# Kernel optimization log

Hardware: AMD Instinct MI355X
Metric: run time of the kernel (lower is better)

Reference implementation:

```python
import jax, jax.numpy as jnp
import numpy as np

WAY, NQ, C, FS = 5, 4096, 64, 5
T = FS * FS            # 25 spatial tokens
EMB = T + 1            # feature_size**2 + feature_proj_dim = 26
HEADS = 2
HD = EMB // HEADS      # 13
SCALE = HD ** -0.5
T_ATTN = 5.0           # args.temperature_attn
TEMP = 0.2             # args.temperature
LN_EPS = 1e-6


def _ln(x, g, b):
    m = x.mean(-1, keepdims=True)
    v = jnp.mean((x - m) ** 2, axis=-1, keepdims=True)
    return (x - m) / jnp.sqrt(v + LN_EPS) * g + b


def _block(x, p):
    # pre-LN transformer block (timm-style), x: (B, T, EMB)
    h = _ln(x, p['ln1_g'], p['ln1_b'])
    qkv = h @ p['qkv_w'].T + p['qkv_b']                       # (B,T,3*EMB)
    B, N, _ = qkv.shape
    qkv = qkv.reshape(B, N, 3, HEADS, HD).transpose(2, 0, 3, 1, 4)
    q, k, v = qkv[0], qkv[1], qkv[2]                          # (B,H,T,hd)
    a = jax.nn.softmax(jnp.einsum('bhqd,bhkd->bhqk', q, k) * SCALE, axis=-1)
    o = jnp.einsum('bhqk,bhkd->bhqd', a, v).transpose(0, 2, 1, 3).reshape(B, N, EMB)
    x = x + o @ p['attn_w'].T + p['attn_b']
    h = _ln(x, p['ln2_g'], p['ln2_b'])
    h = jax.nn.gelu(h @ p['fc1_w'].T + p['fc1_b'], approximate=False)
    return x + h @ p['fc2_w'].T + p['fc2_b']


def _decoder(corr, src, tgt, p):
    # CATs TransformerAggregator, num_hyperpixel=1, depth=1
    # corr: (B,1,T,T); src/tgt: (B,1,T,1) projected features
    pos = jnp.concatenate([
        jnp.broadcast_to(p['pos_x'], (1, 1, FS, FS, EMB // 2)),
        jnp.broadcast_to(p['pos_y'], (1, 1, FS, FS, EMB // 2))], axis=-1).reshape(1, 1, T, EMB)
    B = corr.shape[0]
    x = jnp.concatenate([jnp.swapaxes(corr, -1, -2), tgt], axis=3) + pos
    x = _block(x.reshape(B, T, EMB), p)
    x = (x @ p['dec_w'].T + p['dec_b']).reshape(B, 1, T, T)
    x = jnp.swapaxes(x, -1, -2) + corr            # swap axes for second self-attn pass
    x = jnp.concatenate([x, src], axis=3) + pos
    x = _block(x.reshape(B, T, EMB), p)           # same block weights reused
    x = (x @ p['dec_w'].T + p['dec_b']).reshape(B, 1, T, T) + corr
    return x.mean(axis=1)                         # (B,T,T)


def _forward(spt, qry, proj_w, proj_b, pos_x, pos_y, ln1_g, ln1_b, qkv_w, qkv_b,
             attn_w, attn_b, ln2_g, ln2_b, fc1_w, fc1_b, fc2_w, fc2_b, dec_w, dec_b):
    p = dict(pos_x=pos_x, pos_y=pos_y, ln1_g=ln1_g, ln1_b=ln1_b, qkv_w=qkv_w,
             qkv_b=qkv_b, attn_w=attn_w, attn_b=attn_b, ln2_g=ln2_g, ln2_b=ln2_b,
             fc1_w=fc1_w, fc1_b=fc1_b, fc2_w=fc2_w, fc2_b=fc2_b, dec_w=dec_w, dec_b=dec_b)
    # normalize_feature: subtract channel mean
    spt = spt - spt.mean(axis=1, keepdims=True)
    qry = qry - qry.mean(axis=1, keepdims=True)
    spt_f = jnp.broadcast_to(spt[None], (NQ, WAY, C, FS, FS)).reshape(-1, C, FS, FS)
    qry_f = jnp.broadcast_to(qry[:, None], (NQ, WAY, C, FS, FS)).reshape(-1, C, FS, FS)

    def l2n(x):  # FeatureL2Norm over channel dim
        return x / jnp.sqrt(jnp.sum(x * x, axis=1, keepdims=True) + 1e-6)

    s = l2n(spt_f).reshape(-1, C, T)
    t = l2n(qry_f).reshape(-1, C, T)
    corr = jnp.einsum('bci,bcj->bij', s, t)[:, None]                  # (B,1,T,T)
    sp = (jnp.swapaxes(spt_f.reshape(-1, C, T), 1, 2) @ proj_w.T + proj_b)[:, None]
    tp = (jnp.swapaxes(qry_f.reshape(-1, C, T), 1, 2) @ proj_w.T + proj_b)[:, None]
    refined = _decoder(corr, sp, tp, p)                               # (B,T,T)

    corr_s = refined.reshape(NQ, WAY, T, FS, FS)
    corr_q = refined.reshape(NQ, WAY, FS, FS, T)

    def gnorm(x, axis):  # torch.var is unbiased (ddof=1)
        m = x.mean(axis=axis, keepdims=True)
        v = jnp.var(x, axis=axis, keepdims=True, ddof=1)
        return (x - m) / jnp.sqrt(v + 1e-5)

    corr_s = jax.nn.softmax(gnorm(corr_s, 2) / T_ATTN, axis=2).reshape(NQ, WAY, FS, FS, FS, FS)
    corr_q = jax.nn.softmax(gnorm(corr_q, 4) / T_ATTN, axis=4).reshape(NQ, WAY, FS, FS, FS, FS)
    attn_s = corr_s.sum(axis=(4, 5))                                  # (NQ,WAY,FS,FS)
    attn_q = corr_q.sum(axis=(2, 3))
    spt_att = attn_s[:, :, None] * spt[None]                          # (NQ,WAY,C,FS,FS)
    qry_att = attn_q[:, :, None] * qry[:, None]
    sp_p = spt_att.mean(axis=(-1, -2))                                # (NQ,WAY,C)
    qp_p = qry_att.mean(axis=(-1, -2))
    n1 = jnp.maximum(jnp.linalg.norm(sp_p, axis=-1), 1e-8)
    n2 = jnp.maximum(jnp.linalg.norm(qp_p, axis=-1), 1e-8)
    sim = jnp.sum(sp_p * qp_p, axis=-1) / (n1 * n2)                   # (NQ,WAY)
    return sim / TEMP


def setup_inputs() -> dict:
    key = jax.random.key(0)
    ks = jax.random.split(key, 12)

    def w(i, shape, s=0.02):
        return jax.random.normal(ks[i], shape, jnp.float32) * s

    return {
        'spt': jax.random.normal(ks[0], (WAY, C, FS, FS), jnp.float32),
        'qry': jax.random.normal(ks[1], (NQ, C, FS, FS), jnp.float32),
        'proj_w': w(2, (1, C)), 'proj_b': jnp.zeros((1,), jnp.float32),
        'pos_x': w(3, (1, 1, 1, FS, EMB // 2)),
        'pos_y': w(4, (1, 1, FS, 1, EMB // 2)),
        'ln1_g': jnp.ones((EMB,), jnp.float32), 'ln1_b': jnp.zeros((EMB,), jnp.float32),
        'qkv_w': w(5, (3 * EMB, EMB)), 'qkv_b': jnp.zeros((3 * EMB,), jnp.float32),
        'attn_w': w(6, (EMB, EMB)), 'attn_b': jnp.zeros((EMB,), jnp.float32),
        'ln2_g': jnp.ones((EMB,), jnp.float32), 'ln2_b': jnp.zeros((EMB,), jnp.float32),
        'fc1_w': w(7, (4 * EMB, EMB)), 'fc1_b': jnp.zeros((4 * EMB,), jnp.float32),
        'fc2_w': w(8, (EMB, 4 * EMB)), 'fc2_b': jnp.zeros((EMB,), jnp.float32),
        'dec_w': w(9, (T, EMB)), 'dec_b': jnp.zeros((T,), jnp.float32),
    }


def reference(spt, qry, proj_w, proj_b, pos_x, pos_y, ln1_g, ln1_b, qkv_w, qkv_b,
              attn_w, attn_b, ln2_g, ln2_b, fc1_w, fc1_b, fc2_w, fc2_b, dec_w, dec_b):
    return _forward(spt, qry, proj_w, proj_b, pos_x, pos_y, ln1_g, ln1_b, qkv_w, qkv_b,
                    attn_w, attn_b, ln2_g, ln2_b, fc1_w, fc1_b, fc2_w, fc2_b, dec_w, dec_b)
```

## Files before the change

### kernel.cpp

```cpp
#include <hip/hip_runtime.h>
#include <math.h>

#define WAYS 5
#define NQN 4096
#define NBATCH (NQN*WAYS)
#define SAB 68

#define WS_SC 0
#define WS_RS 8000
#define WS_SP 8125
#define WS_QM 8250
#define WS_QR 110650
#define WS_TP 213050

#define P_L1G 0
#define P_L1B 26
#define P_L2G 52
#define P_L2B 78
#define P_QKVB 104
#define P_ATTB 182
#define P_FC1B 208
#define P_FC2B 312
#define P_DECB 338
#define P_TOT 363

__global__ void prep_spt(const float* __restrict__ spt, const float* __restrict__ proj_w,
                         const float* __restrict__ proj_b, float* __restrict__ ws) {
    int tid = threadIdx.x;
    if (tid >= 125) return;
    int w = tid / 25, i = tid % 25;
    const float* base = spt + w * 1600 + i;
    float s = 0.f;
    for (int c = 0; c < 64; c++) s += base[c * 25];
    float m = s * (1.f / 64.f);
    float ss = 0.f, pj = 0.f;
    for (int c = 0; c < 64; c++) {
        float v = base[c * 25] - m;
        ss += v * v; pj += v * proj_w[c];
        ws[WS_SC + (w * 25 + i) * 64 + c] = v;
    }
    ws[WS_RS + w * 25 + i] = rsqrtf(ss + 1e-6f);
    ws[WS_SP + w * 25 + i] = pj + proj_b[0];
}

__global__ void prep_qry(const float* __restrict__ qry, const float* __restrict__ proj_w,
                         const float* __restrict__ proj_b, float* __restrict__ ws) {
    int idx = blockIdx.x * 256 + threadIdx.x;
    if (idx >= NQN * 25) return;
    int q = idx / 25, j = idx % 25;
    const float* base = qry + q * 1600 + j;
    float s = 0.f;
    for (int c = 0; c < 64; c++) s += base[c * 25];
    float m = s * (1.f / 64.f);
    float ss = 0.f, pj = 0.f;
    for (int c = 0; c < 64; c++) {
        float v = base[c * 25] - m;
        ss += v * v; pj += v * proj_w[c];
    }
    ws[WS_QM + idx] = m;
    ws[WS_QR + idx] = rsqrtf(ss + 1e-6f);
    ws[WS_TP + idx] = pj + proj_b[0];
}

template<int M, int N, int K, int TM, int TN, int SA, int WN, int WK, int SO, int VW,
         bool ADD, bool GELU>
__device__ __forceinline__ void mm(const float* __restrict__ A, const float* __restrict__ W,
                                   const float* __restrict__ bias, float* __restrict__ O,
                                   float scale, int tid) {
    static_assert(M % TM == 0 && N % TN == 0, "tile");
    static_assert(VW == 1 || (WK == 1 && K % VW == 0 && SA % VW == 0 && WN % VW == 0), "vec");
    constexpr int GM = M / TM, GN = N / TN;
    for (int v = tid; v < GM * GN; v += 256) {
        const int m0 = (v / GN) * TM, n0 = (v % GN) * TN;
        float acc[TM][TN];
#pragma unroll
        for (int a = 0; a < TM; a++)
#pragma unroll
            for (int c = 0; c < TN; c++) acc[a][c] = 0.f;

        if constexpr (VW == 4) {
#pragma unroll
            for (int k = 0; k < K; k += 4) {
                float4 av[TM], wv[TN];
#pragma unroll
                for (int a = 0; a < TM; a++) av[a] = *(const float4*)(A + (m0 + a) * SA + k);
#pragma unroll
                for (int c = 0; c < TN; c++) wv[c] = *(const float4*)(W + (n0 + c) * WN + k);
#pragma unroll
                for (int a = 0; a < TM; a++)
#pragma unroll
                    for (int c = 0; c < TN; c++) {
                        acc[a][c] += av[a].x * wv[c].x;
                        acc[a][c] += av[a].y * wv[c].y;
                        acc[a][c] += av[a].z * wv[c].z;
                        acc[a][c] += av[a].w * wv[c].w;
                    }
            }
        } else if constexpr (VW == 2) {
#pragma unroll 4
            for (int k = 0; k < K; k += 2) {
                float2 av[TM], wv[TN];
#pragma unroll
                for (int a = 0; a < TM; a++) av[a] = *(const float2*)(A + (m0 + a) * SA + k);
#pragma unroll
                for (int c = 0; c < TN; c++) wv[c] = *(const float2*)(W + (n0 + c) * WN + k);
#pragma unroll
                for (int a = 0; a < TM; a++)
#pragma unroll
                    for (int c = 0; c < TN; c++) {
                        acc[a][c] += av[a].x * wv[c].x;
                        acc[a][c] += av[a].y * wv[c].y;
                    }
            }
        } else {
#pragma unroll 4
            for (int k = 0; k < K; k++) {
                float av[TM], wv[TN];
#pragma unroll
                for (int a = 0; a < TM; a++) av[a] = A[(m0 + a) * SA + k];
#pragma unroll
                for (int c = 0; c < TN; c++) wv[c] = W[(n0 + c) * WN + k * WK];
#pragma unroll
                for (int a = 0; a < TM; a++)
#pragma unroll
                    for (int c = 0; c < TN; c++) acc[a][c] += av[a] * wv[c];
            }
        }
#pragma unroll
        for (int a = 0; a < TM; a++)
#pragma unroll
            for (int c = 0; c < TN; c++) {
                int n = n0 + c;
                float r = acc[a][c] * scale + (bias ? bias[n] : 0.f);
                if (GELU) r = 0.5f * r * (1.f + erff(r * 0.70710678118654752f));
                if (ADD) O[(m0 + a) * SO + n] += r; else O[(m0 + a) * SO + n] = r;
            }
    }
}

__device__ __forceinline__ void ln_row(const float* __restrict__ x, float* __restrict__ h,
                                       const float* __restrict__ g, const float* __restrict__ bb) {
    float s = 0.f;
#pragma unroll
    for (int e = 0; e < 26; e++) s += x[e];
    float m = s * (1.f / 26.f);
    float vv = 0.f;
#pragma unroll
    for (int e = 0; e < 26; e++) { float d = x[e] - m; vv += d * d; }
    float r = rsqrtf(vv * (1.f / 26.f) + 1e-6f);
#pragma unroll
    for (int e = 0; e < 26; e++) h[e] = (x[e] - m) * r * g[e] + bb[e];
}

__device__ __forceinline__ void xblock(float* __restrict__ xm, float* __restrict__ hm,
                                       float* __restrict__ scr, float* __restrict__ ym,
                                       const float* __restrict__ cpar,
                                       const float* __restrict__ qkv_w,
                                       const float* __restrict__ attn_w,
                                       const float* __restrict__ fc1_w,
                                       const float* __restrict__ fc2_w, int tid) {
    if (tid < 25) ln_row(xm + tid * 26, hm + tid * 26, cpar + P_L1G, cpar + P_L1B);
    __syncthreads();
    mm<25, 78, 26, 5, 3, 26, 26, 1, 78, 2, false, false>(hm, qkv_w, cpar + P_QKVB, scr, 1.f, tid);
    __syncthreads();
    {
        const float SC = 0.27735009811261457f;
        for (int v = tid; v < 250; v += 256) {
            int h = v / 125, r = v % 125;
            int m0 = (r / 25) * 5, j = r % 25;
            const float* kb = scr + j * 78 + 26 + h * 13;
            float acc[5] = {0.f, 0.f, 0.f, 0.f, 0.f};
#pragma unroll
            for (int k = 0; k < 13; k++) {
                float kv = kb[k];
#pragma unroll
                for (int a = 0; a < 5; a++) acc[a] += scr[(m0 + a) * 78 + h * 13 + k] * kv;
            }
            float* orow = ym + h * 625;
#pragma unroll
            for (int a = 0; a < 5; a++) orow[(m0 + a) * 25 + j] = acc[a] * SC;
        }
    }
    __syncthreads();
    if (tid < 50) {
        float* row = ym + (tid / 25) * 625 + (tid % 25) * 25;
        float mx = row[0];
        for (int j = 1; j < 25; j++) mx = fmaxf(mx, row[j]);
        float s = 0.f;
        for (int j = 0; j < 25; j++) { float e = __expf(row[j] - mx); row[j] = e; s += e; }
        float inv = 1.f / s;
        for (int j = 0; j < 25; j++) row[j] *= inv;
    }
    __syncthreads();
    for (int v = tid; v < 130; v += 256) {
        int h = v / 65, r = v % 65;
        int m0 = (r / 13) * 5, n = r % 13;
        const float* P = ym + h * 625;
        float acc[5] = {0.f, 0.f, 0.f, 0.f, 0.f};
#pragma unroll
        for (int k = 0; k < 25; k++) {
            float vv = scr[k * 78 + 52 + h * 13 + n];
#pragma unroll
            for (int a = 0; a < 5; a++) acc[a] += P[(m0 + a) * 25 + k] * vv;
        }
#pragma unroll
        for (int a = 0; a < 5; a++) scr[1950 + (m0 + a) * 26 + h * 13 + n] = acc[a];
    }
    __syncthreads();
    mm<25, 26, 26, 5, 2, 26, 26, 1, 26, 2, true, false>(scr + 1950, attn_w, cpar + P_ATTB, xm, 1.f, tid);
    __syncthreads();
    if (tid < 25) ln_row(xm + tid * 26, hm + tid * 26, cpar + P_L2G, cpar + P_L2B);
    __syncthreads();
    mm<25, 104, 26, 5, 4, 26, 26, 1, 104, 2, false, true>(hm, fc1_w, cpar + P_FC1B, scr, 1.f, tid);
    __syncthreads();
    mm<25, 26, 104, 5, 2, 104, 104, 1, 26, 2, true, false>(scr, fc2_w, cpar + P_FC2B, xm, 1.f, tid);
    __syncthreads();
}

__global__ void __launch_bounds__(256, 4)
fused_kernel(const float* __restrict__ qry, const float* __restrict__ ws,
             const float* __restrict__ pos_x, const float* __restrict__ pos_y,
             const float* __restrict__ qkv_w, const float* __restrict__ qkv_b,
             const float* __restrict__ attn_w, const float* __restrict__ attn_b,
             const float* __restrict__ ln1_g, const float* __restrict__ ln1_b,
             const float* __restrict__ ln2_g, const float* __restrict__ ln2_b,
             const float* __restrict__ fc1_w, const float* __restrict__ fc1_b,
             const float* __restrict__ fc2_w, const float* __restrict__ fc2_b,
             const float* __restrict__ dec_w, const float* __restrict__ dec_b,
             float* __restrict__ out) {
    __shared__ __align__(16) float sc[25 * SAB];
    __shared__ __align__(16) float tcb[25 * SAB];
    __shared__ float rsv[25], rtv[25], spv[25], tpv[25];
    __shared__ __align__(16) float corrm[625];
    __shared__ __align__(16) float xm[650];
    __shared__ __align__(16) float hm[650];
    __shared__ __align__(16) float scr[2600];
    __shared__ __align__(16) float ym[1250];
    __shared__ float asv[25], aqv[25];
    __shared__ __align__(16) float cpar[P_TOT];

    const int b = blockIdx.x, q = b / WAYS, w = b % WAYS, tid = threadIdx.x;

    if (tid < 26) {
        cpar[P_L1G + tid] = ln1_g[tid]; cpar[P_L1B + tid] = ln1_b[tid];
        cpar[P_L2G + tid] = ln2_g[tid]; cpar[P_L2B + tid] = ln2_b[tid];
        cpar[P_ATTB + tid] = attn_b[tid]; cpar[P_FC2B + tid] = fc2_b[tid];
    }
    if (tid < 78) cpar[P_QKVB + tid] = qkv_b[tid];
    if (tid < 104) cpar[P_FC1B + tid] = fc1_b[tid];
    if (tid < 25) cpar[P_DECB + tid] = dec_b[tid];

    for (int e = tid; e < 1600; e += 256) {
        int i = e >> 6, c = e & 63;
        sc[i * SAB + c] = ws[WS_SC + w * 1600 + e] * ws[WS_RS + w * 25 + i];
    }
    if (tid < 25) {
        rsv[tid] = ws[WS_RS + w * 25 + tid];
        spv[tid] = ws[WS_SP + w * 25 + tid];
        rtv[tid] = ws[WS_QR + q * 25 + tid];
        tpv[tid] = ws[WS_TP + q * 25 + tid];
    }
    for (int e = tid; e < 1600; e += 256) {
        int c = e / 25, j = e % 25;
        tcb[j * SAB + c] = (qry[q * 1600 + e] - ws[WS_QM + q * 25 + j]) * ws[WS_QR + q * 25 + j];
    }
    __syncthreads();

    mm<25, 25, 64, 5, 1, SAB, SAB, 1, 25, 4, false, false>(sc, tcb, nullptr, corrm, 1.f, tid);
    __syncthreads();

    for (int e = tid; e < 650; e += 256) {
        int t = e / 26, d = e % 26;
        float p = (d < 13) ? pos_x[(t % 5) * 13 + d] : pos_y[(t / 5) * 13 + (d - 13)];
        float base = (d < 25) ? corrm[d * 25 + t] : tpv[t];
        xm[e] = base + p;
    }
    __syncthreads();

    xblock(xm, hm, scr, ym, cpar, qkv_w, attn_w, fc1_w, fc2_w, tid);

    mm<25, 25, 26, 5, 1, 26, 26, 1, 25, 2, false, false>(xm, dec_w, cpar + P_DECB, ym, 1.f, tid);
    __syncthreads();

    for (int e = tid; e < 650; e += 256) {
        int t = e / 26, d = e % 26;
        float p = (d < 13) ? pos_x[(t % 5) * 13 + d] : pos_y[(t / 5) * 13 + (d - 13)];
        float base = (d < 25) ? (ym[d * 25 + t] + corrm[t * 25 + d]) : spv[t];
        xm[e] = base + p;
    }
    __syncthreads();

    xblock(xm, hm, scr, ym, cpar, qkv_w, attn_w, fc1_w, fc2_w, tid);

    mm<25, 25, 26, 5, 1, 26, 26, 1, 25, 2, false, false>(xm, dec_w, cpar + P_DECB, ym, 1.f, tid);
    __syncthreads();
    for (int e = tid; e < 625; e += 256) ym[e] += corrm[e];
    __syncthreads();

    if (tid < 25) {
        int j = tid;
        float s = 0.f;
        for (int i = 0; i < 25; i++) s += ym[i * 25 + j];
        float m = s * 0.04f;
        float ss = 0.f;
        for (int i = 0; i < 25; i++) { float d = ym[i * 25 + j] - m; ss += d * d; }
        float rinv = rsqrtf(ss * (1.f / 24.f) + 1e-5f) * 0.2f;
        float mx = -1e30f;
        for (int i = 0; i < 25; i++) { float z = (ym[i * 25 + j] - m) * rinv; corrm[i * 25 + j] = z; mx = fmaxf(mx, z); }
        float se = 0.f;
        for (int i = 0; i < 25; i++) { float e2 = __expf(corrm[i * 25 + j] - mx); corrm[i * 25 + j] = e2; se += e2; }
        float inv = 1.f / se;
        for (int i = 0; i < 25; i++) corrm[i * 25 + j] *= inv;
    }
    __syncthreads();
    if (tid < 25) {
        int i = tid; float s = 0.f;
        for (int j = 0; j < 25; j++) s += corrm[i * 25 + j];
        asv[i] = s * 0.04f / rsv[i];
    }
    __syncthreads();
    if (tid < 25) {
        int i = tid;
        float s = 0.f;
        for (int j = 0; j < 25; j++) s += ym[i * 25 + j];
        float m = s * 0.04f;
        float ss = 0.f;
        for (int j = 0; j < 25; j++) { float d = ym[i * 25 + j] - m; ss += d * d; }
        float rinv = rsqrtf(ss * (1.f / 24.f) + 1e-5f) * 0.2f;
        float mx = -1e30f;
        for (int j = 0; j < 25; j++) { float z = (ym[i * 25 + j] - m) * rinv; corrm[i * 25 + j] = z; mx = fmaxf(mx, z); }
        float se = 0.f;
        for (int j = 0; j < 25; j++) { float e2 = __expf(corrm[i * 25 + j] - mx); corrm[i * 25 + j] = e2; se += e2; }
        float inv = 1.f / se;
        for (int j = 0; j < 25; j++) corrm[i * 25 + j] *= inv;
    }
    __syncthreads();
    if (tid < 25) {
        int j = tid; float s = 0.f;
        for (int i = 0; i < 25; i++) s += corrm[i * 25 + j];
        aqv[j] = s * 0.04f / rtv[j];
    }
    __syncthreads();

    if (tid < 64) {
        float s = 0.f;
        for (int i = 0; i < 25; i++) s += asv[i] * sc[i * SAB + tid];
        ym[tid] = s;
        float s2 = 0.f;
        for (int j = 0; j < 25; j++) s2 += aqv[j] * tcb[j * SAB + tid];
        ym[64 + tid] = s2;
    }
    __syncthreads();
    if (tid == 0) {
        float d = 0.f, n1 = 0.f, n2 = 0.f;
        for (int c = 0; c < 64; c++) {
            float a = ym[c], bb2 = ym[64 + c];
            d += a * bb2; n1 += a * a; n2 += bb2 * bb2;
        }
        n1 = fmaxf(sqrtf(n1), 1e-8f);
        n2 = fmaxf(sqrtf(n2), 1e-8f);
        out[b] = d / (n1 * n2) * 5.f;
    }
}

extern "C" void kernel_launch(void* const* d_in, const int* in_sizes, int n_in,
                              void* d_out, int out_size, void* d_ws, size_t ws_size,
                              hipStream_t stream) {
    const float* spt    = (const float*)d_in[0];
    const float* qry    = (const float*)d_in[1];
    const float* proj_w = (const float*)d_in[2];
    const float* proj_b = (const float*)d_in[3];
    const float* pos_x  = (const float*)d_in[4];
    const float* pos_y  = (const float*)d_in[5];
    const float* ln1_g  = (const float*)d_in[6];
    const float* ln1_b  = (const float*)d_in[7];
    const float* qkv_w  = (const float*)d_in[8];
    const float* qkv_b  = (const float*)d_in[9];
    const float* attn_w = (const float*)d_in[10];
    const float* attn_b = (const float*)d_in[11];
    const float* ln2_g  = (const float*)d_in[12];
    const float* ln2_b  = (const float*)d_in[13];
    const float* fc1_w  = (const float*)d_in[14];
    const float* fc1_b  = (const float*)d_in[15];
    const float* fc2_w  = (const float*)d_in[16];
    const float* fc2_b  = (const float*)d_in[17];
    const float* dec_w  = (const float*)d_in[18];
    const float* dec_b  = (const float*)d_in[19];
    float* ws  = (float*)d_ws;
    float* out = (float*)d_out;

    prep_spt<<<1, 128, 0, stream>>>(spt, proj_w, proj_b, ws);
    prep_qry<<<(NQN * 25 + 255) / 256, 256, 0, stream>>>(qry, proj_w, proj_b, ws);
    fused_kernel<<<NBATCH, 256, 0, stream>>>(qry, ws, pos_x, pos_y, qkv_w, qkv_b, attn_w, attn_b,
                                             ln1_g, ln1_b, ln2_g, ln2_b, fc1_w, fc1_b,
                                             fc2_w, fc2_b, dec_w, dec_b, out);
}
```

Baseline: 1.277 ms.

## Map one batch item per wavefront with wave-level sync instead of block barriers

Restructures the fused kernel so each 64-lane wavefront processes one (query, way) item, packing four items per 256-thread block and swapping __syncthreads for wave-local waitcnt/barrier. The attention is fused into a per-row softmax in registers, the matmul helper adds a scalar tail path for leftover tiles, and the MLP and QKV matmuls are split into smaller chunks to fit a 4096-float per-wave LDS slice. Support normalisation is folded into the prep kernel and the final cosine reduction uses shuffles. This aims to cut block-wide barrier overhead and idle threads in the tiny 25x26 ops, at the cost of more work per lane and fewer blocks per CU under the changed launch bounds.

```diff
diff --git a/kernel.cpp b/kernel.cpp
--- a/kernel.cpp
+++ b/kernel.cpp
@@ -4,7 +4,6 @@
 #define WAYS 5
 #define NQN 4096
 #define NBATCH (NQN*WAYS)
-#define SAB 68
 
 #define WS_SC 0
 #define WS_RS 8000
@@ -13,16 +12,7 @@
 #define WS_QR 110650
 #define WS_TP 213050
 
-#define P_L1G 0
-#define P_L1B 26
-#define P_L2G 52
-#define P_L2B 78
-#define P_QKVB 104
-#define P_ATTB 182
-#define P_FC1B 208
-#define P_FC2B 312
-#define P_DECB 338
-#define P_TOT 363
+#define WSYNC() do { asm volatile("s_waitcnt lgkmcnt(0)" ::: "memory"); __builtin_amdgcn_wave_barrier(); } while(0)
 
 __global__ void prep_spt(const float* __restrict__ spt, const float* __restrict__ proj_w,
                          const float* __restrict__ proj_b, float* __restrict__ ws) {
@@ -37,9 +27,11 @@
     for (int c = 0; c < 64; c++) {
         float v = base[c * 25] - m;
         ss += v * v; pj += v * proj_w[c];
-        ws[WS_SC + (w * 25 + i) * 64 + c] = v;
-    }
-    ws[WS_RS + w * 25 + i] = rsqrtf(ss + 1e-6f);
+    }
+    float rinv = rsqrtf(ss + 1e-6f);
+    for (int c = 0; c < 64; c++)
+        ws[WS_SC + (w * 25 + i) * 64 + c] = (base[c * 25] - m) * rinv;
+    ws[WS_RS + w * 25 + i] = rinv;
     ws[WS_SP + w * 25 + i] = pj + proj_b[0];
 }
 
@@ -62,15 +54,20 @@
     ws[WS_TP + idx] = pj + proj_b[0];
 }
 
-template<int M, int N, int K, int TM, int TN, int SA, int WN, int WK, int SO, int VW,
+template<int M, int N, int K, int TM, int TN, int SA, int WN, int SO, int VW,
          bool ADD, bool GELU>
-__device__ __forceinline__ void mm(const float* __restrict__ A, const float* __restrict__ W,
-                                   const float* __restrict__ bias, float* __restrict__ O,
-                                   float scale, int tid) {
+__device__ __forceinline__ void mmw(const float* __restrict__ A, const float* __restrict__ W,
+                                    const float* __restrict__ bias, float* __restrict__ O,
+                                    int lane) {
     static_assert(M % TM == 0 && N % TN == 0, "tile");
-    static_assert(VW == 1 || (WK == 1 && K % VW == 0 && SA % VW == 0 && WN % VW == 0), "vec");
-    constexpr int GM = M / TM, GN = N / TN;
-    for (int v = tid; v < GM * GN; v += 256) {
+    static_assert(K % VW == 0, "vec");
+    constexpr int GM = M / TM, GN = N / TN, ITEMS = GM * GN;
+    constexpr int FULL = (ITEMS / 64) * 64;
+    constexpr int REMO = (ITEMS - FULL) * TM * TN;
+    constexpr bool SCT = (ITEMS > FULL) && (REMO <= 64);
+    constexpr int LIM = SCT ? FULL : ITEMS;
+
+    for (int v = lane; v < LIM; v += 64) {
         const int m0 = (v / GN) * TM, n0 = (v % GN) * TN;
         float acc[TM][TN];
 #pragma unroll
@@ -96,7 +93,7 @@
                         acc[a][c] += av[a].w * wv[c].w;
                     }
             }
-        } else if constexpr (VW == 2) {
+        } else {
 #pragma unroll 4
             for (int k = 0; k < K; k += 2) {
                 float2 av[TM], wv[TN];
@@ -112,29 +109,33 @@
                         acc[a][c] += av[a].y * wv[c].y;
                     }
             }
-        } else {
-#pragma unroll 4
-            for (int k = 0; k < K; k++) {
-                float av[TM], wv[TN];
-#pragma unroll
-                for (int a = 0; a < TM; a++) av[a] = A[(m0 + a) * SA + k];
-#pragma unroll
-                for (int c = 0; c < TN; c++) wv[c] = W[(n0 + c) * WN + k * WK];
-#pragma unroll
-                for (int a = 0; a < TM; a++)
-#pragma unroll
-                    for (int c = 0; c < TN; c++) acc[a][c] += av[a] * wv[c];
-            }
         }
 #pragma unroll
         for (int a = 0; a < TM; a++)
 #pragma unroll
             for (int c = 0; c < TN; c++) {
                 int n = n0 + c;
-                float r = acc[a][c] * scale + (bias ? bias[n] : 0.f);
+                float r = acc[a][c] + (bias ? bias[n] : 0.f);
                 if (GELU) r = 0.5f * r * (1.f + erff(r * 0.70710678118654752f));
                 if (ADD) O[(m0 + a) * SO + n] += r; else O[(m0 + a) * SO + n] = r;
             }
+    }
+    if constexpr (SCT) {
+        if (lane < REMO) {
+            const int t = FULL + lane / (TM * TN), r0 = lane % (TM * TN);
+            const int m = (t / GN) * TM + r0 / TN, n = (t % GN) * TN + r0 % TN;
+            float acc = 0.f;
+#pragma unroll 4
+            for (int k = 0; k < K; k += 2) {
+                float2 a2 = *(const float2*)(A + m * SA + k);
+                float2 w2 = *(const float2*)(W + n * WN + k);
+                acc += a2.x * w2.x;
+                acc += a2.y * w2.y;
+            }
+            float r = acc + (bias ? bias[n] : 0.f);
+            if (GELU) r = 0.5f * r * (1.f + erff(r * 0.70710678118654752f));
+            if (ADD) O[m * SO + n] += r; else O[m * SO + n] = r;
+        }
     }
 }
 
@@ -152,72 +153,7 @@
     for (int e = 0; e < 26; e++) h[e] = (x[e] - m) * r * g[e] + bb[e];
 }
 
-__device__ __forceinline__ void xblock(float* __restrict__ xm, float* __restrict__ hm,
-                                       float* __restrict__ scr, float* __restrict__ ym,
-                                       const float* __restrict__ cpar,
-                                       const float* __restrict__ qkv_w,
-                                       const float* __restrict__ attn_w,
-                                       const float* __restrict__ fc1_w,
-                                       const float* __restrict__ fc2_w, int tid) {
-    if (tid < 25) ln_row(xm + tid * 26, hm + tid * 26, cpar + P_L1G, cpar + P_L1B);
-    __syncthreads();
-    mm<25, 78, 26, 5, 3, 26, 26, 1, 78, 2, false, false>(hm, qkv_w, cpar + P_QKVB, scr, 1.f, tid);
-    __syncthreads();
-    {
-        const float SC = 0.27735009811261457f;
-        for (int v = tid; v < 250; v += 256) {
-            int h = v / 125, r = v % 125;
-            int m0 = (r / 25) * 5, j = r % 25;
-            const float* kb = scr + j * 78 + 26 + h * 13;
-            float acc[5] = {0.f, 0.f, 0.f, 0.f, 0.f};
-#pragma unroll
-            for (int k = 0; k < 13; k++) {
-                float kv = kb[k];
-#pragma unroll
-                for (int a = 0; a < 5; a++) acc[a] += scr[(m0 + a) * 78 + h * 13 + k] * kv;
-            }
-            float* orow = ym + h * 625;
-#pragma unroll
-            for (int a = 0; a < 5; a++) orow[(m0 + a) * 25 + j] = acc[a] * SC;
-        }
-    }
-    __syncthreads();
-    if (tid < 50) {
-        float* row = ym + (tid / 25) * 625 + (tid % 25) * 25;
-        float mx = row[0];
-        for (int j = 1; j < 25; j++) mx = fmaxf(mx, row[j]);
-        float s = 0.f;
-        for (int j = 0; j < 25; j++) { float e = __expf(row[j] - mx); row[j] = e; s += e; }
-        float inv = 1.f / s;
-        for (int j = 0; j < 25; j++) row[j] *= inv;
-    }
-    __syncthreads();
-    for (int v = tid; v < 130; v += 256) {
-        int h = v / 65, r = v % 65;
-        int m0 = (r / 13) * 5, n = r % 13;
-        const float* P = ym + h * 625;
-        float acc[5] = {0.f, 0.f, 0.f, 0.f, 0.f};
-#pragma unroll
-        for (int k = 0; k < 25; k++) {
-            float vv = scr[k * 78 + 52 + h * 13 + n];
-#pragma unroll
-            for (int a = 0; a < 5; a++) acc[a] += P[(m0 + a) * 25 + k] * vv;
-        }
-#pragma unroll
-        for (int a = 0; a < 5; a++) scr[1950 + (m0 + a) * 26 + h * 13 + n] = acc[a];
-    }
-    __syncthreads();
-    mm<25, 26, 26, 5, 2, 26, 26, 1, 26, 2, true, false>(scr + 1950, attn_w, cpar + P_ATTB, xm, 1.f, tid);
-    __syncthreads();
-    if (tid < 25) ln_row(xm + tid * 26, hm + tid * 26, cpar + P_L2G, cpar + P_L2B);
-    __syncthreads();
-    mm<25, 104, 26, 5, 4, 26, 26, 1, 104, 2, false, true>(hm, fc1_w, cpar + P_FC1B, scr, 1.f, tid);
-    __syncthreads();
-    mm<25, 26, 104, 5, 2, 104, 104, 1, 26, 2, true, false>(scr, fc2_w, cpar + P_FC2B, xm, 1.f, tid);
-    __syncthreads();
-}
-
-__global__ void __launch_bounds__(256, 4)
+__global__ void __launch_bounds__(256, 2)
 fused_kernel(const float* __restrict__ qry, const float* __restrict__ ws,
              const float* __restrict__ pos_x, const float* __restrict__ pos_y,
              const float* __restrict__ qkv_w, const float* __restrict__ qkv_b,
@@ -228,138 +164,178 @@
              const float* __restrict__ fc2_w, const float* __restrict__ fc2_b,
              const float* __restrict__ dec_w, const float* __restrict__ dec_b,
              float* __restrict__ out) {
-    __shared__ __align__(16) float sc[25 * SAB];
-    __shared__ __align__(16) float tcb[25 * SAB];
-    __shared__ float rsv[25], rtv[25], spv[25], tpv[25];
-    __shared__ __align__(16) float corrm[625];
-    __shared__ __align__(16) float xm[650];
-    __shared__ __align__(16) float hm[650];
-    __shared__ __align__(16) float scr[2600];
-    __shared__ __align__(16) float ym[1250];
-    __shared__ float asv[25], aqv[25];
-    __shared__ __align__(16) float cpar[P_TOT];
-
-    const int b = blockIdx.x, q = b / WAYS, w = b % WAYS, tid = threadIdx.x;
-
-    if (tid < 26) {
-        cpar[P_L1G + tid] = ln1_g[tid]; cpar[P_L1B + tid] = ln1_b[tid];
-        cpar[P_L2G + tid] = ln2_g[tid]; cpar[P_L2B + tid] = ln2_b[tid];
-        cpar[P_ATTB + tid] = attn_b[tid]; cpar[P_FC2B + tid] = fc2_b[tid];
-    }
-    if (tid < 78) cpar[P_QKVB + tid] = qkv_b[tid];
-    if (tid < 104) cpar[P_FC1B + tid] = fc1_b[tid];
-    if (tid < 25) cpar[P_DECB + tid] = dec_b[tid];
-
-    for (int e = tid; e < 1600; e += 256) {
-        int i = e >> 6, c = e & 63;
-        sc[i * SAB + c] = ws[WS_SC + w * 1600 + e] * ws[WS_RS + w * 25 + i];
-    }
-    if (tid < 25) {
-        rsv[tid] = ws[WS_RS + w * 25 + tid];
-        spv[tid] = ws[WS_SP + w * 25 + tid];
-        rtv[tid] = ws[WS_QR + q * 25 + tid];
-        tpv[tid] = ws[WS_TP + q * 25 + tid];
-    }
-    for (int e = tid; e < 1600; e += 256) {
-        int c = e / 25, j = e % 25;
-        tcb[j * SAB + c] = (qry[q * 1600 + e] - ws[WS_QM + q * 25 + j]) * ws[WS_QR + q * 25 + j];
-    }
-    __syncthreads();
-
-    mm<25, 25, 64, 5, 1, SAB, SAB, 1, 25, 4, false, false>(sc, tcb, nullptr, corrm, 1.f, tid);
-    __syncthreads();
-
-    for (int e = tid; e < 650; e += 256) {
-        int t = e / 26, d = e % 26;
+    __shared__ __align__(16) float lds[4][4096];
+    const int wid = threadIdx.x >> 6, lane = threadIdx.x & 63;
+    const int b = blockIdx.x * 4 + wid, q = b / WAYS, w = b % WAYS;
+
+    float* xm    = lds[wid];
+    float* hm    = xm + 650;
+    float* corrm = xm + 1300;
+    float* sm    = xm + 1925;
+    float* scr   = xm + 1992;
+
+    if (lane < 25) {
+        sm[lane]      = ws[WS_QM + q * 25 + lane];
+        sm[32 + lane] = ws[WS_QR + q * 25 + lane];
+    }
+    WSYNC();
+
+    for (int e = lane; e < 1600; e += 64) {
+        int c = e / 25, j = e - c * 25;
+        scr[j * 68 + c] = (qry[q * 1600 + e] - sm[j]) * sm[32 + j];
+    }
+    WSYNC();
+
+    mmw<25, 25, 64, 5, 1, 64, 68, 25, 4, false, false>(ws + WS_SC + w * 1600, scr, nullptr, corrm, lane);
+    WSYNC();
+
+    for (int e = lane; e < 650; e += 64) {
+        int t = e / 26, d = e - t * 26;
         float p = (d < 13) ? pos_x[(t % 5) * 13 + d] : pos_y[(t / 5) * 13 + (d - 13)];
-        float base = (d < 25) ? corrm[d * 25 + t] : tpv[t];
+        float base = (d < 25) ? corrm[d * 25 + t] : ws[WS_TP + q * 25 + t];
         xm[e] = base + p;
     }
-    __syncthreads();
-
-    xblock(xm, hm, scr, ym, cpar, qkv_w, attn_w, fc1_w, fc2_w, tid);
-
-    mm<25, 25, 26, 5, 1, 26, 26, 1, 25, 2, false, false>(xm, dec_w, cpar + P_DECB, ym, 1.f, tid);
-    __syncthreads();
-
-    for (int e = tid; e < 650; e += 256) {
-        int t = e / 26, d = e % 26;
-        float p = (d < 13) ? pos_x[(t % 5) * 13 + d] : pos_y[(t / 5) * 13 + (d - 13)];
-        float base = (d < 25) ? (ym[d * 25 + t] + corrm[t * 25 + d]) : spv[t];
-        xm[e] = base + p;
-    }
-    __syncthreads();
-
-    xblock(xm, hm, scr, ym, cpar, qkv_w, attn_w, fc1_w, fc2_w, tid);
-
-    mm<25, 25, 26, 5, 1, 26, 26, 1, 25, 2, false, false>(xm, dec_w, cpar + P_DECB, ym, 1.f, tid);
-    __syncthreads();
-    for (int e = tid; e < 625; e += 256) ym[e] += corrm[e];
-    __syncthreads();
-
-    if (tid < 25) {
-        int j = tid;
+    WSYNC();
+
+    for (int it = 0; it < 2; ++it) {
+        if (lane < 25) ln_row(xm + lane * 26, hm + lane * 26, ln1_g, ln1_b);
+        WSYNC();
+        mmw<25, 26, 26, 5, 2, 26, 26, 84, 2, false, false>(hm, qkv_w,        qkv_b,      scr,      lane);
+        mmw<25, 26, 26, 5, 2, 26, 26, 84, 2, false, false>(hm, qkv_w + 676,  qkv_b + 26, scr + 28, lane);
+        mmw<25, 26, 26, 5, 2, 26, 26, 84, 2, false, false>(hm, qkv_w + 1352, qkv_b + 52, scr + 56, lane);
+        WSYNC();
+        if (lane < 50) {
+            int h = lane / 25, i = lane - h * 25;
+            const float* qb = scr + i * 84 + h * 13;
+            float qv[13];
+#pragma unroll
+            for (int k = 0; k < 13; k++) qv[k] = qb[k];
+            float P[25];
+            float mx = -1e30f;
+#pragma unroll
+            for (int j = 0; j < 25; j++) {
+                const float* kb = scr + j * 84 + 28 + h * 13;
+                float a = 0.f;
+#pragma unroll
+                for (int k = 0; k < 13; k++) a += qv[k] * kb[k];
+                a *= 0.27735009811261457f;
+                P[j] = a; mx = fmaxf(mx, a);
+            }
+            float s = 0.f;
+#pragma unroll
+            for (int j = 0; j < 25; j++) { P[j] = __expf(P[j] - mx); s += P[j]; }
+            float inv = 1.f / s;
+            float o[13];
+#pragma unroll
+            for (int n = 0; n < 13; n++) o[n] = 0.f;
+#pragma unroll
+            for (int k = 0; k < 25; k++) {
+                const float* vb = scr + k * 84 + 56 + h * 13;
+                float p = P[k];
+#pragma unroll
+                for (int n = 0; n < 13; n++) o[n] += p * vb[n];
+            }
+            float* ob = hm + i * 26 + h * 13;
+#pragma unroll
+            for (int n = 0; n < 13; n++) ob[n] = o[n] * inv;
+        }
+        WSYNC();
+        mmw<25, 26, 26, 5, 2, 26, 26, 26, 2, true, false>(hm, attn_w, attn_b, xm, lane);
+        WSYNC();
+        if (lane < 25) ln_row(xm + lane * 26, hm + lane * 26, ln2_g, ln2_b);
+        WSYNC();
+        mmw<25, 52, 26, 5, 4, 26, 26, 52, 2, false, true>(hm, fc1_w, fc1_b, scr, lane);
+        WSYNC();
+        mmw<25, 26, 52, 5, 2, 52, 104, 26, 2, true, false>(scr, fc2_w, fc2_b, xm, lane);
+        WSYNC();
+        mmw<25, 52, 26, 5, 4, 26, 26, 52, 2, false, true>(hm, fc1_w + 1352, fc1_b + 52, scr, lane);
+        WSYNC();
+        mmw<25, 26, 52, 5, 2, 52, 104, 26, 2, true, false>(scr, fc2_w + 52, nullptr, xm, lane);
+        WSYNC();
+        mmw<25, 25, 26, 5, 1, 26, 26, 25, 2, false, false>(xm, dec_w, dec_b, scr, lane);
+        WSYNC();
+        if (it == 0) {
+            for (int e = lane; e < 650; e += 64) {
+                int t = e / 26, d = e - t * 26;
+                float p = (d < 13) ? pos_x[(t % 5) * 13 + d] : pos_y[(t / 5) * 13 + (d - 13)];
+                float base = (d < 25) ? (scr[d * 25 + t] + corrm[t * 25 + d]) : ws[WS_SP + w * 25 + t];
+                xm[e] = base + p;
+            }
+            WSYNC();
+        }
+    }
+
+    for (int e = lane; e < 625; e += 64) scr[e] += corrm[e];
+    WSYNC();
+
+    if (lane < 25) {
+        int j = lane;
         float s = 0.f;
-        for (int i = 0; i < 25; i++) s += ym[i * 25 + j];
+        for (int i = 0; i < 25; i++) s += scr[i * 25 + j];
         float m = s * 0.04f;
         float ss = 0.f;
-        for (int i = 0; i < 25; i++) { float d = ym[i * 25 + j] - m; ss += d * d; }
+        for (int i = 0; i < 25; i++) { float d = scr[i * 25 + j] - m; ss += d * d; }
         float rinv = rsqrtf(ss * (1.f / 24.f) + 1e-5f) * 0.2f;
         float mx = -1e30f;
-        for (int i = 0; i < 25; i++) { float z = (ym[i * 25 + j] - m) * rinv; corrm[i * 25 + j] = z; mx = fmaxf(mx, z); }
+        for (int i = 0; i < 25; i++) { float z = (scr[i * 25 + j] - m) * rinv; corrm[i * 25 + j] = z; mx = fmaxf(mx, z); }
         float se = 0.f;
         for (int i = 0; i < 25; i++) { float e2 = __expf(corrm[i * 25 + j] - mx); corrm[i * 25 + j] = e2; se += e2; }
         float inv = 1.f / se;
         for (int i = 0; i < 25; i++) corrm[i * 25 + j] *= inv;
     }
-    __syncthreads();
-    if (tid < 25) {
-        int i = tid; float s = 0.f;
+    WSYNC();
+    if (lane < 25) {
+        int i = lane; float s = 0.f;
         for (int j = 0; j < 25; j++) s += corrm[i * 25 + j];
-        asv[i] = s * 0.04f / rsv[i];
-    }
-    __syncthreads();
-    if (tid < 25) {
-        int i = tid;
+        hm[i] = s * 0.04f / ws[WS_RS + w * 25 + i];
+    }
+    WSYNC();
+    if (lane < 25) {
+        int i = lane;
         float s = 0.f;
-        for (int j = 0; j < 25; j++) s += ym[i * 25 + j];
+        for (int j = 0; j < 25; j++) s += scr[i * 25 + j];
         float m = s * 0.04f;
         float ss = 0.f;
-        for (int j = 0; j < 25; j++) { float d = ym[i * 25 + j] - m; ss += d * d; }
+        for (int j = 0; j < 25; j++) { float d = scr[i * 25 + j] - m; ss += d * d; }
         float rinv = rsqrtf(ss * (1.f / 24.f) + 1e-5f) * 0.2f;
         float mx = -1e30f;
-        for (int j = 0; j < 25; j++) { float z = (ym[i * 25 + j] - m) * rinv; corrm[i * 25 + j] = z; mx = fmaxf(mx, z); }
+        for (int j = 0; j < 25; j++) { float z = (scr[i * 25 + j] - m) * rinv; corrm[i * 25 + j] = z; mx = fmaxf(mx, z); }
         float se = 0.f;
         for (int j = 0; j < 25; j++) { float e2 = __expf(corrm[i * 25 + j] - mx); corrm[i * 25 + j] = e2; se += e2; }
         float inv = 1.f / se;
         for (int j = 0; j < 25; j++) corrm[i * 25 + j] *= inv;
     }
-    __syncthreads();
-    if (tid < 25) {
-        int j = tid; float s = 0.f;
+    WSYNC();
+    if (lane < 25) {
+        int j = lane; float s = 0.f;
         for (int i = 0; i < 25; i++) s += corrm[i * 25 + j];
-        aqv[j] = s * 0.04f / rtv[j];
-    }
-    __syncthreads();
-
-    if (tid < 64) {
-        float s = 0.f;
-        for (int i = 0; i < 25; i++) s += asv[i] * sc[i * SAB + tid];
-        ym[tid] = s;
-        float s2 = 0.f;
-        for (int j = 0; j < 25; j++) s2 += aqv[j] * tcb[j * SAB + tid];
-        ym[64 + tid] = s2;
-    }
-    __syncthreads();
-    if (tid == 0) {
-        float d = 0.f, n1 = 0.f, n2 = 0.f;
-        for (int c = 0; c < 64; c++) {
-            float a = ym[c], bb2 = ym[64 + c];
-            d += a * bb2; n1 += a * a; n2 += bb2 * bb2;
-        }
-        n1 = fmaxf(sqrtf(n1), 1e-8f);
-        n2 = fmaxf(sqrtf(n2), 1e-8f);
-        out[b] = d / (n1 * n2) * 5.f;
+        hm[32 + j] = s * 0.04f / sm[32 + j];
+    }
+    WSYNC();
+
+    for (int e = lane; e < 1600; e += 64) {
+        int c = e / 25, j = e - c * 25;
+        scr[e] = (qry[q * 1600 + e] - sm[j]) * sm[32 + j];
+    }
+    WSYNC();
+
+    {
+        float sv = 0.f, qv2 = 0.f;
+        const float* snb = ws + WS_SC + w * 1600 + lane;
+        for (int i = 0; i < 25; i++) sv  += hm[i]      * snb[i * 64];
+        for (int j = 0; j < 25; j++) qv2 += hm[32 + j] * scr[lane * 25 + j];
+        float d = sv * qv2, n1 = sv * sv, n2 = qv2 * qv2;
+#pragma unroll
+        for (int msk = 32; msk >= 1; msk >>= 1) {
+            d  += __shfl_xor(d,  msk);
+            n1 += __shfl_xor(n1, msk);
+            n2 += __shfl_xor(n2, msk);
+        }
+        if (lane == 0) {
+            n1 = fmaxf(sqrtf(n1), 1e-8f);
+            n2 = fmaxf(sqrtf(n2), 1e-8f);
+            out[b] = d / (n1 * n2) * 5.f;
+        }
     }
 }
 
@@ -391,7 +367,7 @@
 
     prep_spt<<<1, 128, 0, stream>>>(spt, proj_w, proj_b, ws);
     prep_qry<<<(NQN * 25 + 255) / 256, 256, 0, stream>>>(qry, proj_w, proj_b, ws);
-    fused_kernel<<<NBATCH, 256, 0, stream>>>(qry, ws, pos_x, pos_y, qkv_w, qkv_b, attn_w, attn_b,
-                                             ln1_g, ln1_b, ln2_g, ln2_b, fc1_w, fc1_b,
-                                             fc2_w, fc2_b, dec_w, dec_b, out);
-}
+    fused_kernel<<<NBATCH / 4, 256, 0, stream>>>(qry, ws, pos_x, pos_y, qkv_w, qkv_b, attn_w, attn_b,
+                                                 ln1_g, ln1_b, ln2_g, ln2_b, fc1_w, fc1_b,
+                                                 fc2_w, fc2_b, dec_w, dec_b, out);
+}
```

Result: no change. 1.302 ms (+1.9%).
